# Kernel tuning notes

Measured on AMD Instinct MI355X. Metric: run time of the kernel, lower is better.

The kernel has to match this reference:

```python
import jax, jax.numpy as jnp
import numpy as np

D_MODEL = 1024
NHEADS = 16
D_K = D_MODEL // NHEADS


def setup_inputs() -> dict:
    key = jax.random.key(0)
    ks = jax.random.split(key, 5)
    s = 1.0 / np.sqrt(D_MODEL)
    x = jax.random.normal(ks[0], (4, 2048, D_MODEL), dtype=jnp.float32)
    Wq = jax.random.normal(ks[1], (D_MODEL, D_MODEL), dtype=jnp.float32) * s
    Wk = jax.random.normal(ks[2], (D_MODEL, D_MODEL), dtype=jnp.float32) * s
    Wv = jax.random.normal(ks[3], (D_MODEL, D_MODEL), dtype=jnp.float32) * s
    Wo = jax.random.normal(ks[4], (D_MODEL, D_MODEL), dtype=jnp.float32) * s
    z = jnp.zeros((D_MODEL,), dtype=jnp.float32)
    return {"x": x, "Wq": Wq, "bq": z, "Wk": Wk, "bk": z,
            "Wv": Wv, "bv": z, "Wo": Wo, "bo": z}


def reference(x, Wq, bq, Wk, bk, Wv, bv, Wo, bo):
    B, S, _ = x.shape
    # nn.Linear: y = x @ W^T + b  (weights stored [out, in])
    def proj(W, b):
        h = x @ W.T + b                       # [B, S, D]
        return h.reshape(B, S, NHEADS, D_K).transpose(0, 2, 1, 3)  # [B, H, S, d_k]
    Q = proj(Wq, bq)
    K = proj(Wk, bk)
    V = proj(Wv, bv)
    scores = jnp.einsum("bhqd,bhkd->bhqk", Q, K) / jnp.sqrt(jnp.float32(D_K))
    attn = jax.nn.softmax(scores, axis=-1)    # dropout p=0.0 -> identity
    ctx = jnp.einsum("bhqk,bhkd->bhqd", attn, V)
    ctx = ctx.transpose(0, 2, 1, 3).reshape(B, S, D_MODEL)
    return ctx @ Wo.T + bo
```

## Files before the change

### kernel.cpp

```cpp
#include <hip/hip_runtime.h>
#include <stdint.h>
#include <stddef.h>

typedef _Float16 f16;
typedef f16 f16x8 __attribute__((ext_vector_type(8)));
typedef f16 f16x4 __attribute__((ext_vector_type(4)));
typedef f16 f16x2 __attribute__((ext_vector_type(2)));
typedef float f32x4 __attribute__((ext_vector_type(4)));
typedef float f32x16 __attribute__((ext_vector_type(16)));
typedef unsigned int u32x4 __attribute__((ext_vector_type(4)));

#define SEQ 2048
#define DM 1024
#define NH 16
#define DK 64
#define MTOT 8192

__device__ __forceinline__ void gload16(const f16* g, f16* l) {
    __builtin_amdgcn_global_load_lds(
        (const __attribute__((address_space(1))) uint32_t*)g,
        (__attribute__((address_space(3))) uint32_t*)l,
        16, 0, 0);
}

__device__ __forceinline__ unsigned int pkrtz(float a, float b) {
    return __builtin_bit_cast(unsigned int, __builtin_amdgcn_cvt_pkrtz(a, b));
}

__device__ __forceinline__ void plswap(unsigned int& a, unsigned int& b) {
    auto r = __builtin_amdgcn_permlane32_swap(a, b, false, false);
    unsigned int n0 = r[0], n1 = r[1];
    a = n0; b = n1;
}
__device__ __forceinline__ float xhalf_sum(float x) {
    unsigned int ux = __builtin_bit_cast(unsigned int, x);
    auto r = __builtin_amdgcn_permlane32_swap(ux, ux, false, false);
    unsigned int n0 = r[0], n1 = r[1];
    return __builtin_bit_cast(float, n0) + __builtin_bit_cast(float, n1);
}

__global__ void cvt_f32_f16(const float* __restrict__ src, f16* __restrict__ dst, int n) {
    int i = (blockIdx.x * 256 + threadIdx.x) * 8;
    if (i >= n) return;
    float4 a = *(const float4*)(src + i);
    float4 b = *(const float4*)(src + i + 4);
    f16x8 o = {(f16)a.x, (f16)a.y, (f16)a.z, (f16)a.w,
               (f16)b.x, (f16)b.y, (f16)b.z, (f16)b.w};
    *(f16x8*)(dst + i) = o;
}

__global__ void cvt4(const float* __restrict__ s0, const float* __restrict__ s1,
                     const float* __restrict__ s2, const float* __restrict__ s3,
                     f16* __restrict__ d0, f16* __restrict__ d1,
                     f16* __restrict__ d2, f16* __restrict__ d3) {
    int y = blockIdx.y;
    const float* s = y == 0 ? s0 : y == 1 ? s1 : y == 2 ? s2 : s3;
    f16* d = y == 0 ? d0 : y == 1 ? d1 : y == 2 ? d2 : d3;
    int i = (blockIdx.x * 256 + threadIdx.x) * 8;
    float4 a = *(const float4*)(s + i);
    float4 b = *(const float4*)(s + i + 4);
    f16x8 o = {(f16)a.x, (f16)a.y, (f16)a.z, (f16)a.w,
               (f16)b.x, (f16)b.y, (f16)b.z, (f16)b.w};
    *(f16x8*)(d + i) = o;
}

__device__ __forceinline__
void gemm_body(const f16* __restrict__ A, const f16* __restrict__ Bw,
               const float* __restrict__ bias, void* __restrict__ outp,
               int mode, float oscale, int bm, int bn, f16* As, f16* Bs) {
    const int tid = threadIdx.x;
    const int w = tid >> 6, lane = tid & 63;
    const int g = lane >> 4, c16 = lane & 15;
    const int wr = w >> 1, wc = w & 1;
    const int r8 = lane >> 3, co = (lane & 7) * 8;

    f32x4 acc[4][4] = {};

    const f16* Ab = A + (size_t)bm * 128 * DM;
    const f16* Bb = Bw + (size_t)bn * 128 * DM;

    for (int kt = 0; kt < DM / 64; ++kt) {
        if (kt) __syncthreads();
        const f16* As_src = Ab + kt * 64;
        const f16* Bs_src = Bb + kt * 64;
#pragma unroll
        for (int i = 0; i < 4; ++i) {
            int c = 4 * w + i;
            gload16(As_src + (size_t)(c * 8 + r8) * DM + co, As + c * 512);
            gload16(Bs_src + (size_t)(c * 8 + r8) * DM + co, Bs + c * 512);
        }
        __syncthreads();
#pragma unroll
        for (int kk = 0; kk < 2; ++kk) {
            f16x8 a[4], b[4];
            const int ko = kk * 32 + g * 8;
#pragma unroll
            for (int m = 0; m < 4; ++m)
                a[m] = *(const f16x8*)(As + (wr * 64 + m * 16 + c16) * 64 + ko);
#pragma unroll
            for (int n = 0; n < 4; ++n)
                b[n] = *(const f16x8*)(Bs + (wc * 64 + n * 16 + c16) * 64 + ko);
#pragma unroll
            for (int m = 0; m < 4; ++m)
#pragma unroll
                for (int n = 0; n < 4; ++n)
                    acc[m][n] = __builtin_amdgcn_mfma_f32_16x16x32_f16(a[m], b[n], acc[m][n], 0, 0, 0);
        }
    }

#pragma unroll
    for (int m = 0; m < 4; ++m) {
#pragma unroll
        for (int n = 0; n < 4; ++n) {
            const int col = bn * 128 + wc * 64 + n * 16 + c16;
            const float bv = bias[col];
            const int row0 = bm * 128 + wr * 64 + m * 16 + g * 4;
            if (mode == 1) {
                int b = row0 >> 11, s0 = row0 & 2047;
                int h = col >> 6, d = col & 63;
                f16x4 pv;
#pragma unroll
                for (int j = 0; j < 4; ++j) pv[j] = (f16)((acc[m][n][j] + bv) * oscale);
                *(f16x4*)((f16*)outp + (((size_t)(b * NH + h) * DK + d) * SEQ + s0)) = pv;
            } else if (mode == 0) {
#pragma unroll
                for (int j = 0; j < 4; ++j) {
                    int row = row0 + j;
                    int b = row >> 11, s = row & 2047;
                    int h = col >> 6, d = col & 63;
                    ((f16*)outp)[((size_t)(b * NH + h) * SEQ + s) * DK + d] =
                        (f16)((acc[m][n][j] + bv) * oscale);
                }
            } else {
#pragma unroll
                for (int j = 0; j < 4; ++j) {
                    int row = row0 + j;
                    ((float*)outp)[(size_t)row * DM + col] = acc[m][n][j] + bv;
                }
            }
        }
    }
}

__global__ __launch_bounds__(256, 2)
void gemm_qkv(const f16* __restrict__ A,
              const f16* __restrict__ W0, const f16* __restrict__ W1, const f16* __restrict__ W2,
              const float* __restrict__ b0, const float* __restrict__ b1, const float* __restrict__ b2,
              f16* __restrict__ Qo, f16* __restrict__ Ko, f16* __restrict__ Vto) {
    __shared__ __align__(16) f16 As[128 * 64];
    __shared__ __align__(16) f16 Bs[128 * 64];
    const int bid = blockIdx.x;
    const int wg = (bid & 7) * 192 + (bid >> 3);
    const int which = wg >> 9;
    const int t = wg & 511;
    const f16* Bw = which == 0 ? W0 : which == 1 ? W1 : W2;
    const float* bias = which == 0 ? b0 : which == 1 ? b1 : b2;
    void* outp = which == 0 ? (void*)Qo : which == 1 ? (void*)Ko : (void*)Vto;
    const int mode = (which == 2) ? 1 : 0;
    const float oscale = (which == 0) ? 0.18033688f : 1.0f;
    gemm_body(A, Bw, bias, outp, mode, oscale, t >> 3, t & 7, As, Bs);
}

__global__ __launch_bounds__(256, 2)
void gemm_out(const f16* __restrict__ A, const f16* __restrict__ Wo,
              const float* __restrict__ bias, float* __restrict__ outp) {
    __shared__ __align__(16) f16 As[128 * 64];
    __shared__ __align__(16) f16 Bs[128 * 64];
    const int bid = blockIdx.x;
    const int wg = (bid & 7) * 64 + (bid >> 3);
    gemm_body(A, Wo, bias, outp, 2, 1.0f, wg >> 3, wg & 7, As, Bs);
}

__global__ __launch_bounds__(128, 2)
void attn(const f16* __restrict__ Qg, const f16* __restrict__ Kg,
          const f16* __restrict__ Vg, f16* __restrict__ ctx) {
    __shared__ __align__(16) f16 Ks[2][64 * 64];
    __shared__ __align__(16) f16 Vs[2][64 * 64];
    const int tid = threadIdx.x;
    const int w = tid >> 6, lane = tid & 63;
    const int q31 = lane & 31, hi = lane >> 5;
    const int bid = blockIdx.x;
    const int wg = (bid & 7) * 128 + (bid >> 3);
    const int bh = wg >> 4, qt = wg & 15;
    const int b = bh >> 4, h = bh & 15;
    const f16* Qp = Qg + (size_t)bh * SEQ * DK;
    const f16* Kp = Kg + (size_t)bh * SEQ * DK;
    const f16* Vp = Vg + (size_t)bh * DK * SEQ;
    const int q0w = qt * 128 + w * 64;

    f16x8 qfA[4], qfB[4];
#pragma unroll
    for (int ks4 = 0; ks4 < 4; ++ks4) {
        qfA[ks4] = *(const f16x8*)(Qp + (size_t)(q0w + q31) * DK + ks4 * 16 + hi * 8);
        qfB[ks4] = *(const f16x8*)(Qp + (size_t)(q0w + 32 + q31) * DK + ks4 * 16 + hi * 8);
    }

    const f32x16 z = {};
    const f16x2 one2 = {(f16)1.0f, (f16)1.0f};
    f32x16 OA0 = {}, OA1 = {}, OB0 = {}, OB1 = {};
    float lrA = 0.f, lrB = 0.f;

    const int srow = lane >> 3;
    const int scol = lane & 7;

#define STAGE(bufi, kvoff)                                                        \
    {                                                                             \
        _Pragma("unroll")                                                         \
        for (int i_ = 0; i_ < 4; ++i_) {                                          \
            int c_ = w * 4 + i_;                                                  \
            int row_ = c_ * 8 + srow;                                             \
            int csw_ = (scol ^ (row_ & 7)) * 8;                                   \
            gload16(Kp + (size_t)((kvoff) + row_) * DK + csw_, &Ks[bufi][c_ * 512]); \
            gload16(Vp + (size_t)row_ * SEQ + (kvoff) + csw_, &Vs[bufi][c_ * 512]);  \
        }                                                                         \
    }

    STAGE(0, 0);
    __syncthreads();
    int cur = 0;
    const int fsw = (q31 & 7) << 4;

    for (int kv = 0; kv < SEQ; kv += 64) {
        if (kv + 64 < SEQ) STAGE(cur ^ 1, kv + 64);

        const char* Kb = (const char*)Ks[cur];
        f32x16 sA0, sA1, sB0, sB1;
        __builtin_amdgcn_s_setprio(1);
#pragma unroll
        for (int ks4 = 0; ks4 < 4; ++ks4) {
            const int off = (ks4 * 32 + hi * 16) ^ fsw;
            f16x8 kf0 = *(const f16x8*)(Kb + q31 * 128 + off);
            f16x8 kf1 = *(const f16x8*)(Kb + (32 + q31) * 128 + off);
            if (ks4 == 0) {
                sA0 = __builtin_amdgcn_mfma_f32_32x32x16_f16(kf0, qfA[0], z, 0, 0, 0);
                sA1 = __builtin_amdgcn_mfma_f32_32x32x16_f16(kf1, qfA[0], z, 0, 0, 0);
                sB0 = __builtin_amdgcn_mfma_f32_32x32x16_f16(kf0, qfB[0], z, 0, 0, 0);
                sB1 = __builtin_amdgcn_mfma_f32_32x32x16_f16(kf1, qfB[0], z, 0, 0, 0);
            } else {
                sA0 = __builtin_amdgcn_mfma_f32_32x32x16_f16(kf0, qfA[ks4], sA0, 0, 0, 0);
                sA1 = __builtin_amdgcn_mfma_f32_32x32x16_f16(kf1, qfA[ks4], sA1, 0, 0, 0);
                sB0 = __builtin_amdgcn_mfma_f32_32x32x16_f16(kf0, qfB[ks4], sB0, 0, 0, 0);
                sB1 = __builtin_amdgcn_mfma_f32_32x32x16_f16(kf1, qfB[ks4], sB1, 0, 0, 0);
            }
        }
        __builtin_amdgcn_s_setprio(0);

        f16x8 paA[4], paB[4];
        auto soft = [&](f32x16& t0, f32x16& t1, f16x8* pa, float& lr) {
#pragma unroll
            for (int r = 0; r < 16; ++r) {
                t0[r] = __builtin_amdgcn_exp2f(t0[r]);
                t1[r] = __builtin_amdgcn_exp2f(t1[r]);
            }
            float ls0 = 0.f, ls1 = 0.f;
            unsigned int u[8];
#pragma unroll
            for (int kb = 0; kb < 2; ++kb) {
                const f32x16& sp = kb ? t1 : t0;
#pragma unroll
                for (int j = 0; j < 4; ++j) {
                    u[2 * j]     = pkrtz(sp[4 * j], sp[4 * j + 1]);
                    u[2 * j + 1] = pkrtz(sp[4 * j + 2], sp[4 * j + 3]);
                }
#pragma unroll
                for (int j = 0; j < 4; ++j) {
                    ls0 = __builtin_amdgcn_fdot2(__builtin_bit_cast(f16x2, u[2 * j]), one2, ls0, false);
                    ls1 = __builtin_amdgcn_fdot2(__builtin_bit_cast(f16x2, u[2 * j + 1]), one2, ls1, false);
                }
                plswap(u[0], u[2]);
                plswap(u[1], u[3]);
                plswap(u[4], u[6]);
                plswap(u[5], u[7]);
                u32x4 t0w = {u[0], u[1], u[2], u[3]};
                u32x4 t1w = {u[4], u[5], u[6], u[7]};
                pa[kb * 2]     = __builtin_bit_cast(f16x8, t0w);
                pa[kb * 2 + 1] = __builtin_bit_cast(f16x8, t1w);
            }
            lr += xhalf_sum(ls0 + ls1);
        };
        soft(sA0, sA1, paA, lrA);
        soft(sB0, sB1, paB, lrB);

        const char* Vb = (const char*)Vs[cur];
        __builtin_amdgcn_s_setprio(1);
#pragma unroll
        for (int ksl = 0; ksl < 4; ++ksl) {
            const int off = (ksl * 32 + hi * 16) ^ fsw;
            f16x8 vf0 = *(const f16x8*)(Vb + q31 * 128 + off);
            f16x8 vf1 = *(const f16x8*)(Vb + (32 + q31) * 128 + off);
            OA0 = __builtin_amdgcn_mfma_f32_32x32x16_f16(vf0, paA[ksl], OA0, 0, 0, 0);
            OA1 = __builtin_amdgcn_mfma_f32_32x32x16_f16(vf1, paA[ksl], OA1, 0, 0, 0);
            OB0 = __builtin_amdgcn_mfma_f32_32x32x16_f16(vf0, paB[ksl], OB0, 0, 0, 0);
            OB1 = __builtin_amdgcn_mfma_f32_32x32x16_f16(vf1, paB[ksl], OB1, 0, 0, 0);
        }
        __builtin_amdgcn_s_setprio(0);

        __syncthreads();
        cur ^= 1;
    }
#undef STAGE

    f16* tw = (f16*)&Ks[0][0] + w * 4096;
    {
        const float rlA = 1.f / lrA;
        const float rlB = 1.f / lrB;
#pragma unroll
        for (int f = 0; f < 2; ++f) {
            const float rl = f ? rlB : rlA;
            char* twf = (char*)tw + f * 4096;
#pragma unroll
            for (int dblk = 0; dblk < 2; ++dblk) {
                const f32x16& Op = f ? (dblk ? OB1 : OB0) : (dblk ? OA1 : OA0);
#pragma unroll
                for (int rp = 0; rp < 8; ++rp) {
                    int r = 2 * rp;
                    int d0 = dblk * 32 + (r & 3) + 8 * (r >> 2) + 4 * hi;
                    unsigned int uv = pkrtz(Op[r] * rl, Op[r + 1] * rl);
                    *(unsigned int*)(twf + q31 * 128 + ((d0 * 2) ^ ((q31 & 7) << 4))) = uv;
                }
            }
        }
    }
#pragma unroll
    for (int p4 = 0; p4 < 8; ++p4) {
        int qq = p4 * 8 + (lane >> 3), ch = lane & 7;
        f16x8 v = *(const f16x8*)((const char*)tw + (qq >> 5) * 4096 + (qq & 31) * 128 +
                                  ((ch * 16) ^ ((qq & 7) << 4)));
        *(f16x8*)(ctx + (size_t)(b * SEQ + q0w + qq) * DM + h * DK + ch * 8) = v;
    }
}

extern "C" void kernel_launch(void* const* d_in, const int* in_sizes, int n_in,
                              void* d_out, int out_size, void* d_ws, size_t ws_size,
                              hipStream_t stream) {
    const float* x  = (const float*)d_in[0];
    const float* Wq = (const float*)d_in[1];
    const float* bq = (const float*)d_in[2];
    const float* Wk = (const float*)d_in[3];
    const float* bk = (const float*)d_in[4];
    const float* Wv = (const float*)d_in[5];
    const float* bv = (const float*)d_in[6];
    const float* Wo = (const float*)d_in[7];
    const float* bo = (const float*)d_in[8];

    f16* ws  = (f16*)d_ws;
    f16* xh  = ws;
    f16* Wqh = ws + (size_t)8 * 1024 * 1024;
    f16* Wkh = Wqh + 1024 * 1024;
    f16* Wvh = Wkh + 1024 * 1024;
    f16* Woh = Wvh + 1024 * 1024;
    f16* Vtb = Woh + 1024 * 1024;
    f16* Qb = (f16*)d_out;
    f16* Kb = Qb + (size_t)8 * 1024 * 1024;
    f16* ctx = xh;

    const int nx = MTOT * DM;
    cvt_f32_f16<<<nx / 8 / 256, 256, 0, stream>>>(x, xh, nx);
    cvt4<<<dim3(512, 4), 256, 0, stream>>>(Wq, Wk, Wv, Wo, Wqh, Wkh, Wvh, Woh);

    gemm_qkv<<<1536, 256, 0, stream>>>(xh, Wqh, Wkh, Wvh, bq, bk, bv, Qb, Kb, Vtb);

    attn<<<1024, 128, 0, stream>>>(Qb, Kb, Vtb, ctx);

    gemm_out<<<512, 256, 0, stream>>>(ctx, Woh, bo, (float*)d_out);
}
```

Measured before the change: 195.7 us.

## Widen attention blocks to four waves and interleave softmax halves with PV MFMAs

```diff
diff --git a/kernel.cpp b/kernel.cpp
--- a/kernel.cpp
+++ b/kernel.cpp
@@ -171,7 +171,7 @@
     gemm_body(A, Wo, bias, outp, 2, 1.0f, wg >> 3, wg & 7, As, Bs);
 }
 
-__global__ __launch_bounds__(128, 2)
+__global__ __launch_bounds__(256, 2)
 void attn(const f16* __restrict__ Qg, const f16* __restrict__ Kg,
           const f16* __restrict__ Vg, f16* __restrict__ ctx) {
     __shared__ __align__(16) f16 Ks[2][64 * 64];
@@ -180,13 +180,13 @@
     const int w = tid >> 6, lane = tid & 63;
     const int q31 = lane & 31, hi = lane >> 5;
     const int bid = blockIdx.x;
-    const int wg = (bid & 7) * 128 + (bid >> 3);
-    const int bh = wg >> 4, qt = wg & 15;
+    const int wg = (bid & 7) * 64 + (bid >> 3);
+    const int bh = wg >> 3, qt = wg & 7;
     const int b = bh >> 4, h = bh & 15;
     const f16* Qp = Qg + (size_t)bh * SEQ * DK;
     const f16* Kp = Kg + (size_t)bh * SEQ * DK;
     const f16* Vp = Vg + (size_t)bh * DK * SEQ;
-    const int q0w = qt * 128 + w * 64;
+    const int q0w = qt * 256 + w * 64;
 
     f16x8 qfA[4], qfB[4];
 #pragma unroll
@@ -206,8 +206,8 @@
 #define STAGE(bufi, kvoff)                                                        \
     {                                                                             \
         _Pragma("unroll")                                                         \
-        for (int i_ = 0; i_ < 4; ++i_) {                                          \
-            int c_ = w * 4 + i_;                                                  \
+        for (int i_ = 0; i_ < 2; ++i_) {                                          \
+            int c_ = w * 2 + i_;                                                  \
             int row_ = c_ * 8 + srow;                                             \
             int csw_ = (scol ^ (row_ & 7)) * 8;                                   \
             gload16(Kp + (size_t)((kvoff) + row_) * DK + csw_, &Ks[bufi][c_ * 512]); \
@@ -220,71 +220,72 @@
     int cur = 0;
     const int fsw = (q31 & 7) << 4;
 
+    auto soft32 = [&](f32x16& sp, f16x8& paLo, f16x8& paHi, float& ls) {
+#pragma unroll
+        for (int r = 0; r < 16; ++r) sp[r] = __builtin_amdgcn_exp2f(sp[r]);
+        unsigned int u[8];
+#pragma unroll
+        for (int j = 0; j < 4; ++j) {
+            u[2 * j]     = pkrtz(sp[4 * j], sp[4 * j + 1]);
+            u[2 * j + 1] = pkrtz(sp[4 * j + 2], sp[4 * j + 3]);
+        }
+        float ls0 = 0.f, ls1 = 0.f;
+#pragma unroll
+        for (int j = 0; j < 4; ++j) {
+            ls0 = __builtin_amdgcn_fdot2(__builtin_bit_cast(f16x2, u[2 * j]), one2, ls0, false);
+            ls1 = __builtin_amdgcn_fdot2(__builtin_bit_cast(f16x2, u[2 * j + 1]), one2, ls1, false);
+        }
+        ls += ls0 + ls1;
+        plswap(u[0], u[2]);
+        plswap(u[1], u[3]);
+        plswap(u[4], u[6]);
+        plswap(u[5], u[7]);
+        u32x4 t0w = {u[0], u[1], u[2], u[3]};
+        u32x4 t1w = {u[4], u[5], u[6], u[7]};
+        paLo = __builtin_bit_cast(f16x8, t0w);
+        paHi = __builtin_bit_cast(f16x8, t1w);
+    };
+
     for (int kv = 0; kv < SEQ; kv += 64) {
         if (kv + 64 < SEQ) STAGE(cur ^ 1, kv + 64);
 
         const char* Kb = (const char*)Ks[cur];
+        const char* Vb = (const char*)Vs[cur];
         f32x16 sA0, sA1, sB0, sB1;
-        __builtin_amdgcn_s_setprio(1);
+
 #pragma unroll
         for (int ks4 = 0; ks4 < 4; ++ks4) {
             const int off = (ks4 * 32 + hi * 16) ^ fsw;
             f16x8 kf0 = *(const f16x8*)(Kb + q31 * 128 + off);
+            if (ks4 == 0) {
+                sA0 = __builtin_amdgcn_mfma_f32_32x32x16_f16(kf0, qfA[0], z, 0, 0, 0);
+                sB0 = __builtin_amdgcn_mfma_f32_32x32x16_f16(kf0, qfB[0], z, 0, 0, 0);
+            } else {
+                sA0 = __builtin_amdgcn_mfma_f32_32x32x16_f16(kf0, qfA[ks4], sA0, 0, 0, 0);
+                sB0 = __builtin_amdgcn_mfma_f32_32x32x16_f16(kf0, qfB[ks4], sB0, 0, 0, 0);
+            }
+        }
+#pragma unroll
+        for (int ks4 = 0; ks4 < 4; ++ks4) {
+            const int off = (ks4 * 32 + hi * 16) ^ fsw;
             f16x8 kf1 = *(const f16x8*)(Kb + (32 + q31) * 128 + off);
             if (ks4 == 0) {
-                sA0 = __builtin_amdgcn_mfma_f32_32x32x16_f16(kf0, qfA[0], z, 0, 0, 0);
                 sA1 = __builtin_amdgcn_mfma_f32_32x32x16_f16(kf1, qfA[0], z, 0, 0, 0);
-                sB0 = __builtin_amdgcn_mfma_f32_32x32x16_f16(kf0, qfB[0], z, 0, 0, 0);
                 sB1 = __builtin_amdgcn_mfma_f32_32x32x16_f16(kf1, qfB[0], z, 0, 0, 0);
             } else {
-                sA0 = __builtin_amdgcn_mfma_f32_32x32x16_f16(kf0, qfA[ks4], sA0, 0, 0, 0);
                 sA1 = __builtin_amdgcn_mfma_f32_32x32x16_f16(kf1, qfA[ks4], sA1, 0, 0, 0);
-                sB0 = __builtin_amdgcn_mfma_f32_32x32x16_f16(kf0, qfB[ks4], sB0, 0, 0, 0);
                 sB1 = __builtin_amdgcn_mfma_f32_32x32x16_f16(kf1, qfB[ks4], sB1, 0, 0, 0);
             }
         }
-        __builtin_amdgcn_s_setprio(0);
 
         f16x8 paA[4], paB[4];
-        auto soft = [&](f32x16& t0, f32x16& t1, f16x8* pa, float& lr) {
-#pragma unroll
-            for (int r = 0; r < 16; ++r) {
-                t0[r] = __builtin_amdgcn_exp2f(t0[r]);
-                t1[r] = __builtin_amdgcn_exp2f(t1[r]);
-            }
-            float ls0 = 0.f, ls1 = 0.f;
-            unsigned int u[8];
-#pragma unroll
-            for (int kb = 0; kb < 2; ++kb) {
-                const f32x16& sp = kb ? t1 : t0;
-#pragma unroll
-                for (int j = 0; j < 4; ++j) {
-                    u[2 * j]     = pkrtz(sp[4 * j], sp[4 * j + 1]);
-                    u[2 * j + 1] = pkrtz(sp[4 * j + 2], sp[4 * j + 3]);
-                }
-#pragma unroll
-                for (int j = 0; j < 4; ++j) {
-                    ls0 = __builtin_amdgcn_fdot2(__builtin_bit_cast(f16x2, u[2 * j]), one2, ls0, false);
-                    ls1 = __builtin_amdgcn_fdot2(__builtin_bit_cast(f16x2, u[2 * j + 1]), one2, ls1, false);
-                }
-                plswap(u[0], u[2]);
-                plswap(u[1], u[3]);
-                plswap(u[4], u[6]);
-                plswap(u[5], u[7]);
-                u32x4 t0w = {u[0], u[1], u[2], u[3]};
-                u32x4 t1w = {u[4], u[5], u[6], u[7]};
-                pa[kb * 2]     = __builtin_bit_cast(f16x8, t0w);
-                pa[kb * 2 + 1] = __builtin_bit_cast(f16x8, t1w);
-            }
-            lr += xhalf_sum(ls0 + ls1);
-        };
-        soft(sA0, sA1, paA, lrA);
-        soft(sB0, sB1, paB, lrB);
-
-        const char* Vb = (const char*)Vs[cur];
-        __builtin_amdgcn_s_setprio(1);
-#pragma unroll
-        for (int ksl = 0; ksl < 4; ++ksl) {
+        float lsA = 0.f, lsB = 0.f;
+
+        soft32(sA0, paA[0], paA[1], lsA);
+        soft32(sB0, paB[0], paB[1], lsB);
+
+#pragma unroll
+        for (int ksl = 0; ksl < 2; ++ksl) {
             const int off = (ksl * 32 + hi * 16) ^ fsw;
             f16x8 vf0 = *(const f16x8*)(Vb + q31 * 128 + off);
             f16x8 vf1 = *(const f16x8*)(Vb + (32 + q31) * 128 + off);
@@ -293,7 +294,23 @@
             OB0 = __builtin_amdgcn_mfma_f32_32x32x16_f16(vf0, paB[ksl], OB0, 0, 0, 0);
             OB1 = __builtin_amdgcn_mfma_f32_32x32x16_f16(vf1, paB[ksl], OB1, 0, 0, 0);
         }
-        __builtin_amdgcn_s_setprio(0);
+
+        soft32(sA1, paA[2], paA[3], lsA);
+        soft32(sB1, paB[2], paB[3], lsB);
+
+#pragma unroll
+        for (int ksl = 2; ksl < 4; ++ksl) {
+            const int off = (ksl * 32 + hi * 16) ^ fsw;
+            f16x8 vf0 = *(const f16x8*)(Vb + q31 * 128 + off);
+            f16x8 vf1 = *(const f16x8*)(Vb + (32 + q31) * 128 + off);
+            OA0 = __builtin_amdgcn_mfma_f32_32x32x16_f16(vf0, paA[ksl], OA0, 0, 0, 0);
+            OA1 = __builtin_amdgcn_mfma_f32_32x32x16_f16(vf1, paA[ksl], OA1, 0, 0, 0);
+            OB0 = __builtin_amdgcn_mfma_f32_32x32x16_f16(vf0, paB[ksl], OB0, 0, 0, 0);
+            OB1 = __builtin_amdgcn_mfma_f32_32x32x16_f16(vf1, paB[ksl], OB1, 0, 0, 0);
+        }
+
+        lrA += xhalf_sum(lsA);
+        lrB += xhalf_sum(lsB);
 
         __syncthreads();
         cur ^= 1;
@@ -360,7 +377,7 @@
 
     gemm_qkv<<<1536, 256, 0, stream>>>(xh, Wqh, Wkh, Wvh, bq, bk, bv, Qb, Kb, Vtb);
 
-    attn<<<1024, 128, 0, stream>>>(Qb, Kb, Vtb, ctx);
+    attn<<<512, 256, 0, stream>>>(Qb, Kb, Vtb, ctx);
 
     gemm_out<<<512, 256, 0, stream>>>(ctx, Woh, bo, (float*)d_out);
 }
```

Measured after the change: 190.1 us. -2.9%, faster.
